# Kernel optimization log

Hardware: AMD Instinct MI355X
Metric: run time of the kernel (lower is better)

The kernel has to match this reference:

```python
import jax, jax.numpy as jnp
import numpy as np

INPUT_DIM, HIDDEN, OUT_DIM = 7, 64, 4


def _lstm_layer(x_seq, W_ih, W_hh, b_ih, b_hh):
    """Single LSTM layer, batch_first x_seq [B,T,D] -> [B,T,H]. PyTorch gate order i,f,g,o."""
    B = x_seq.shape[0]
    H = W_hh.shape[1]
    # Precompute input projection for all timesteps (hoist GEMM out of the scan).
    x_proj = jnp.einsum('btd,gd->btg', x_seq, W_ih) + b_ih + b_hh  # [B,T,4H]

    def step(carry, xt):
        h, c = carry
        gates = xt + h @ W_hh.T  # [B,4H]
        i, f, g, o = jnp.split(gates, 4, axis=-1)
        i = jax.nn.sigmoid(i)
        f = jax.nn.sigmoid(f)
        g = jnp.tanh(g)
        o = jax.nn.sigmoid(o)
        c = f * c + i * g
        h = o * jnp.tanh(c)
        return (h, c), h

    h0 = jnp.zeros((B, H), x_seq.dtype)
    c0 = jnp.zeros((B, H), x_seq.dtype)
    (_, _), hs = jax.lax.scan(step, (h0, c0), jnp.swapaxes(x_proj, 0, 1))  # hs [T,B,H]
    return jnp.swapaxes(hs, 0, 1)  # [B,T,H]


def setup_inputs() -> dict:
    key = jax.random.key(0)
    ks = jax.random.split(key, 12)
    s = 0.1  # init scale ~ 1/sqrt(hidden)
    x = jax.random.normal(ks[0], (4096, 512, INPUT_DIM), dtype=jnp.float32)
    W_ih0 = jax.random.normal(ks[1], (4 * HIDDEN, INPUT_DIM), dtype=jnp.float32) * s
    W_hh0 = jax.random.normal(ks[2], (4 * HIDDEN, HIDDEN), dtype=jnp.float32) * s
    b_ih0 = jax.random.normal(ks[3], (4 * HIDDEN,), dtype=jnp.float32) * s
    b_hh0 = jax.random.normal(ks[4], (4 * HIDDEN,), dtype=jnp.float32) * s
    W_ih1 = jax.random.normal(ks[5], (4 * HIDDEN, HIDDEN), dtype=jnp.float32) * s
    W_hh1 = jax.random.normal(ks[6], (4 * HIDDEN, HIDDEN), dtype=jnp.float32) * s
    b_ih1 = jax.random.normal(ks[7], (4 * HIDDEN,), dtype=jnp.float32) * s
    b_hh1 = jax.random.normal(ks[8], (4 * HIDDEN,), dtype=jnp.float32) * s
    W_fc = jax.random.normal(ks[9], (OUT_DIM, HIDDEN), dtype=jnp.float32) * s
    b_fc = jax.random.normal(ks[10], (OUT_DIM,), dtype=jnp.float32) * s
    return {"x": x, "W_ih0": W_ih0, "W_hh0": W_hh0, "b_ih0": b_ih0, "b_hh0": b_hh0,
            "W_ih1": W_ih1, "W_hh1": W_hh1, "b_ih1": b_ih1, "b_hh1": b_hh1,
            "W_fc": W_fc, "b_fc": b_fc}


def reference(x, W_ih0, W_hh0, b_ih0, b_hh0, W_ih1, W_hh1, b_ih1, b_hh1, W_fc, b_fc):
    h1 = _lstm_layer(x, W_ih0, W_hh0, b_ih0, b_hh0)   # [B,T,H]
    h2 = _lstm_layer(h1, W_ih1, W_hh1, b_ih1, b_hh1)  # [B,T,H]
    last = h2[:, -1, :]                               # [B,H]
    return last @ W_fc.T + b_fc                       # [B,4]
```

## Files before the change

kernel.cpp:

```cpp
#include <hip/hip_runtime.h>

#define T_SEQ 512
#define HID 64
#define MB 16
#define NTHREADS 1024
#define A1STR 104
#define A2STR 104

typedef __attribute__((ext_vector_type(8))) short short8;
typedef __attribute__((ext_vector_type(4))) float floatx4;

#define LOG2E 1.4426950408889634f

__device__ __forceinline__ short f2bf_rne(float v) {
  unsigned u = __float_as_uint(v);
  return (short)((u + 0x7FFFu + ((u >> 16) & 1u)) >> 16);
}
__device__ __forceinline__ float rcp_(float x) { return __builtin_amdgcn_rcpf(x); }
__device__ __forceinline__ float exp2_(float x) { return __builtin_amdgcn_exp2f(x); }

__device__ __forceinline__ float gate_h(const floatx4 p, float& c) {
  float A = exp2_(-p[0]);
  float F = exp2_(-p[1]);
  float G = exp2_(p[2]);
  float O = exp2_(-p[3]);
  float ig = (G - 1.f) * rcp_((1.f + A) * (G + 1.f));
  c = rcp_(1.f + F) * c + ig;
  float C = exp2_((2.f * LOG2E) * c);
  return (C - 1.f) * rcp_((1.f + O) * (C + 1.f));
}

__device__ __forceinline__ int uofp(int p) {
  return (p & ~7) + ((p & 7) >> 1) + ((p & 1) << 2);
}

__device__ __forceinline__ short w1elem(int k, int n, float wsc,
                                        const float* __restrict__ Wih0,
                                        const float* __restrict__ Whh0) {
  float v;
  if      (k < 64) { v = Whh0[n*64 + uofp(k)]; }
  else if (k < 71) { v = Wih0[n*7 + (k - 64)]; }
  else return (short)0;
  return f2bf_rne(v * wsc);
}
__device__ __forceinline__ short w2elem(int k, int n, float wsc,
                                        const float* __restrict__ Wih1,
                                        const float* __restrict__ Whh1) {
  float v;
  if (k < 64) { v = Wih1[n*64 + uofp(k)]; }
  else        { v = Whh1[n*64 + uofp(k - 64)]; }
  return f2bf_rne(v * wsc);
}

#define MFMA(A, B, C) __builtin_amdgcn_mfma_f32_16x16x32_bf16((A), (B), (C), 0, 0, 0)

#define PACK2(ha, hb)                                                        \
  ((unsigned)(unsigned short)f2bf_rne(ha) |                                  \
   ((unsigned)(unsigned short)f2bf_rne(hb) << 16))

__global__ __launch_bounds__(NTHREADS, 4) void lstm_fused(
    const float* __restrict__ x,
    const float* __restrict__ Wih0, const float* __restrict__ Whh0,
    const float* __restrict__ bih0, const float* __restrict__ bhh0,
    const float* __restrict__ Wih1, const float* __restrict__ Whh1,
    const float* __restrict__ bih1, const float* __restrict__ bhh1,
    const float* __restrict__ Wfc,  const float* __restrict__ bfc,
    float* __restrict__ out)
{
  __shared__ __align__(16) short A1[2][MB][A1STR];
  __shared__ __align__(16) short A2[2][MB][A2STR];
  __shared__ float h2f[MB][HID + 4];

  const int tid  = threadIdx.x;
  const int lane = tid & 63;
  const int wave = tid >> 6;
  const int wl   = wave & 7;
  const bool isL1 = wave < 8;
  const int l15  = lane & 15;
  const int quad = lane >> 4;
  const int quad8= quad * 8;
  const int g4   = l15 & 3;
  const int b0   = blockIdx.x * MB;
  const int u0   = wl*8 + quad;
  const int u1   = u0 + 4;
  const int hpos = wl*8 + 2*quad;
  const int n0   = g4*64 + (wl*8 + (l15 >> 2));
  const int n1   = n0 + 4;
  const float wsc = (g4 == 2) ? 2.f * LOG2E : LOG2E;

  for (int i = tid; i < 2*MB*A1STR/2; i += NTHREADS) ((unsigned*)A1)[i] = 0u;
  for (int i = tid; i < 2*MB*A2STR/2; i += NTHREADS) ((unsigned*)A2)[i] = 0u;

  const float* bi_ = isL1 ? bih0 : bih1;
  const float* bh_ = isL1 ? bhh0 : bhh1;
  floatx4 bia, bib;
  #pragma unroll
  for (int g = 0; g < 4; ++g) {
    float ws = (g == 2) ? 2.f * LOG2E : LOG2E;
    bia[g] = (bi_[g*64 + u0] + bh_[g*64 + u0]) * ws;
    bib[g] = (bi_[g*64 + u1] + bh_[g*64 + u1]) * ws;
  }

  const int xd   = lane & 31;
  const int xrow = 2*wl + (lane >> 5);
  const bool xact = isL1 && (xd < 7);
  const float* xbase = x + ((size_t)(b0 + xrow) * T_SEQ) * 7 + xd;
  float xcur = 0.f;
  if (xact) {
    A1[0][xrow][64 + xd] = f2bf_rne(xbase[0]);
    xcur = xbase[7];
  }

  short8 WA[4], WB[4];
  if (isL1) {
    #pragma unroll
    for (int ks = 0; ks < 3; ++ks) {
      short8 fa, fb;
      #pragma unroll
      for (int jj = 0; jj < 8; ++jj) {
        fa[jj] = w1elem(ks*32 + quad8 + jj, n0, wsc, Wih0, Whh0);
        fb[jj] = w1elem(ks*32 + quad8 + jj, n1, wsc, Wih0, Whh0);
      }
      WA[ks] = fa; WB[ks] = fb;
    }
  } else {
    #pragma unroll
    for (int ks = 0; ks < 4; ++ks) {
      short8 fa, fb;
      #pragma unroll
      for (int jj = 0; jj < 8; ++jj) {
        fa[jj] = w2elem(ks*32 + quad8 + jj, n0, wsc, Wih1, Whh1);
        fb[jj] = w2elem(ks*32 + quad8 + jj, n1, wsc, Wih1, Whh1);
      }
      WA[ks] = fa; WB[ks] = fb;
    }
  }
  __syncthreads();

  float ca = 0.f, cb = 0.f;

#define STEP_X(NXT, XT)                                                      \
    if (xact) {                                                              \
      A1[NXT][xrow][64 + xd] = f2bf_rne(xcur);                               \
      xcur = xbase[7 * (XT)];                                                \
    }

#define STEP_FULL(CUR, NXT, IT)                                              \
  {                                                                          \
    if (isL1) {                                                              \
      int xt_ = (IT) + 2; if (xt_ > T_SEQ - 1) xt_ = T_SEQ - 1;              \
      STEP_X(NXT, xt_)                                                       \
      short8 hf0 = *(const short8*)&A1[CUR][l15][     quad8];                \
      short8 hf1 = *(const short8*)&A1[CUR][l15][32 + quad8];                \
      short8 hfx = *(const short8*)&A1[CUR][l15][64 + quad8];                \
      floatx4 pa = bia, pb = bib;                                            \
      pa = MFMA(WA[0], hf0, pa);  pb = MFMA(WB[0], hf0, pb);                 \
      pa = MFMA(WA[1], hf1, pa);  pb = MFMA(WB[1], hf1, pb);                 \
      pa = MFMA(WA[2], hfx, pa);  pb = MFMA(WB[2], hfx, pb);                 \
      float ha = gate_h(pa, ca);                                             \
      float hb = gate_h(pb, cb);                                             \
      *(unsigned*)&A1[NXT][l15][hpos] = PACK2(ha, hb);                       \
    } else {                                                                 \
      short8 hf0 = *(const short8*)&A1[CUR][l15][     quad8];                \
      short8 hf1 = *(const short8*)&A1[CUR][l15][32 + quad8];                \
      short8 h20 = *(const short8*)&A2[CUR][l15][     quad8];                \
      short8 h21 = *(const short8*)&A2[CUR][l15][32 + quad8];                \
      floatx4 pa = bia, pb = bib;                                            \
      pa = MFMA(WA[0], hf0, pa);  pb = MFMA(WB[0], hf0, pb);                 \
      pa = MFMA(WA[1], hf1, pa);  pb = MFMA(WB[1], hf1, pb);                 \
      pa = MFMA(WA[2], h20, pa);  pb = MFMA(WB[2], h20, pb);                 \
      pa = MFMA(WA[3], h21, pa);  pb = MFMA(WB[3], h21, pb);                 \
      float ha = gate_h(pa, ca);                                             \
      float hb = gate_h(pb, cb);                                             \
      *(unsigned*)&A2[NXT][l15][hpos] = PACK2(ha, hb);                       \
    }                                                                        \
    __syncthreads();                                                         \
  }

  {
    if (isL1) {
      STEP_X(1, 2)
      short8 hf0 = *(const short8*)&A1[0][l15][     quad8];
      short8 hf1 = *(const short8*)&A1[0][l15][32 + quad8];
      short8 hfx = *(const short8*)&A1[0][l15][64 + quad8];
      floatx4 pa = bia, pb = bib;
      pa = MFMA(WA[0], hf0, pa);  pb = MFMA(WB[0], hf0, pb);
      pa = MFMA(WA[1], hf1, pa);  pb = MFMA(WB[1], hf1, pb);
      pa = MFMA(WA[2], hfx, pa);  pb = MFMA(WB[2], hfx, pb);
      float ha = gate_h(pa, ca);
      float hb = gate_h(pb, cb);
      *(unsigned*)&A1[1][l15][hpos] = PACK2(ha, hb);
    }
    __syncthreads();
  }

  #pragma unroll 1
  for (int k = 0; k < 255; ++k) {
    STEP_FULL(1, 0, 2*k + 1)
    STEP_FULL(0, 1, 2*k + 2)
  }
  STEP_FULL(1, 0, 511)

  {
    if (!isL1) {
      short8 hf0 = *(const short8*)&A1[0][l15][     quad8];
      short8 hf1 = *(const short8*)&A1[0][l15][32 + quad8];
      short8 h20 = *(const short8*)&A2[0][l15][     quad8];
      short8 h21 = *(const short8*)&A2[0][l15][32 + quad8];
      floatx4 pa = bia, pb = bib;
      pa = MFMA(WA[0], hf0, pa);  pb = MFMA(WB[0], hf0, pb);
      pa = MFMA(WA[1], hf1, pa);  pb = MFMA(WB[1], hf1, pb);
      pa = MFMA(WA[2], h20, pa);  pb = MFMA(WB[2], h20, pb);
      pa = MFMA(WA[3], h21, pa);  pb = MFMA(WB[3], h21, pb);
      h2f[l15][u0] = gate_h(pa, ca);
      h2f[l15][u1] = gate_h(pb, cb);
    }
    __syncthreads();
  }

  if (tid < MB * 4) {
    int bbf = tid >> 2, o = tid & 3;
    float acc = bfc[o];
    #pragma unroll 8
    for (int kk = 0; kk < HID; ++kk) acc += h2f[bbf][kk] * Wfc[o*HID + kk];
    out[(size_t)(b0 + bbf) * 4 + o] = acc;
  }
}

extern "C" void kernel_launch(void* const* d_in, const int* in_sizes, int n_in,
                              void* d_out, int out_size, void* d_ws, size_t ws_size,
                              hipStream_t stream) {
  const float* x    = (const float*)d_in[0];
  const float* Wih0 = (const float*)d_in[1];
  const float* Whh0 = (const float*)d_in[2];
  const float* bih0 = (const float*)d_in[3];
  const float* bhh0 = (const float*)d_in[4];
  const float* Wih1 = (const float*)d_in[5];
  const float* Whh1 = (const float*)d_in[6];
  const float* bih1 = (const float*)d_in[7];
  const float* bhh1 = (const float*)d_in[8];
  const float* Wfc  = (const float*)d_in[9];
  const float* bfc  = (const float*)d_in[10];
  (void)d_ws; (void)ws_size; (void)n_in; (void)out_size;

  const int B = in_sizes[0] / (T_SEQ * 7);
  dim3 grid(B / MB);
  lstm_fused<<<grid, NTHREADS, 0, stream>>>(x, Wih0, Whh0, bih0, bhh0,
                                            Wih1, Whh1, bih1, bhh1, Wfc, bfc,
                                            (float*)d_out);
}
```

Measured before the change: 438.5 us.

## Merge layer-1 and layer-2 waves so each wave computes both LSTM layers

```diff
diff --git a/kernel.cpp b/kernel.cpp
--- a/kernel.cpp
+++ b/kernel.cpp
@@ -3,7 +3,7 @@
 #define T_SEQ 512
 #define HID 64
 #define MB 16
-#define NTHREADS 1024
+#define NTHREADS 512
 #define A1STR 104
 #define A2STR 104
 
@@ -74,36 +74,34 @@
   const int tid  = threadIdx.x;
   const int lane = tid & 63;
   const int wave = tid >> 6;
-  const int wl   = wave & 7;
-  const bool isL1 = wave < 8;
   const int l15  = lane & 15;
   const int quad = lane >> 4;
   const int quad8= quad * 8;
   const int g4   = l15 & 3;
   const int b0   = blockIdx.x * MB;
-  const int u0   = wl*8 + quad;
+  const int u0   = wave*8 + quad;
   const int u1   = u0 + 4;
-  const int hpos = wl*8 + 2*quad;
-  const int n0   = g4*64 + (wl*8 + (l15 >> 2));
+  const int hpos = wave*8 + 2*quad;
+  const int n0   = g4*64 + (wave*8 + (l15 >> 2));
   const int n1   = n0 + 4;
   const float wsc = (g4 == 2) ? 2.f * LOG2E : LOG2E;
 
   for (int i = tid; i < 2*MB*A1STR/2; i += NTHREADS) ((unsigned*)A1)[i] = 0u;
   for (int i = tid; i < 2*MB*A2STR/2; i += NTHREADS) ((unsigned*)A2)[i] = 0u;
 
-  const float* bi_ = isL1 ? bih0 : bih1;
-  const float* bh_ = isL1 ? bhh0 : bhh1;
-  floatx4 bia, bib;
+  floatx4 b1a, b1b, b2a, b2b;
   #pragma unroll
   for (int g = 0; g < 4; ++g) {
     float ws = (g == 2) ? 2.f * LOG2E : LOG2E;
-    bia[g] = (bi_[g*64 + u0] + bh_[g*64 + u0]) * ws;
-    bib[g] = (bi_[g*64 + u1] + bh_[g*64 + u1]) * ws;
+    b1a[g] = (bih0[g*64 + u0] + bhh0[g*64 + u0]) * ws;
+    b1b[g] = (bih0[g*64 + u1] + bhh0[g*64 + u1]) * ws;
+    b2a[g] = (bih1[g*64 + u0] + bhh1[g*64 + u0]) * ws;
+    b2b[g] = (bih1[g*64 + u1] + bhh1[g*64 + u1]) * ws;
   }
 
   const int xd   = lane & 31;
-  const int xrow = 2*wl + (lane >> 5);
-  const bool xact = isL1 && (xd < 7);
+  const int xrow = 2*wave + (lane >> 5);
+  const bool xact = (xd < 7);
   const float* xbase = x + ((size_t)(b0 + xrow) * T_SEQ) * 7 + xd;
   float xcur = 0.f;
   if (xact) {
@@ -111,33 +109,30 @@
     xcur = xbase[7];
   }
 
-  short8 WA[4], WB[4];
-  if (isL1) {
+  short8 W1f[3][2], W2f[4][2];
+  #pragma unroll
+  for (int ks = 0; ks < 3; ++ks) {
+    short8 fa, fb;
     #pragma unroll
-    for (int ks = 0; ks < 3; ++ks) {
-      short8 fa, fb;
-      #pragma unroll
-      for (int jj = 0; jj < 8; ++jj) {
-        fa[jj] = w1elem(ks*32 + quad8 + jj, n0, wsc, Wih0, Whh0);
-        fb[jj] = w1elem(ks*32 + quad8 + jj, n1, wsc, Wih0, Whh0);
-      }
-      WA[ks] = fa; WB[ks] = fb;
+    for (int jj = 0; jj < 8; ++jj) {
+      fa[jj] = w1elem(ks*32 + quad8 + jj, n0, wsc, Wih0, Whh0);
+      fb[jj] = w1elem(ks*32 + quad8 + jj, n1, wsc, Wih0, Whh0);
     }
-  } else {
+    W1f[ks][0] = fa; W1f[ks][1] = fb;
+  }
+  #pragma unroll
+  for (int ks = 0; ks < 4; ++ks) {
+    short8 fa, fb;
     #pragma unroll
-    for (int ks = 0; ks < 4; ++ks) {
-      short8 fa, fb;
-      #pragma unroll
-      for (int jj = 0; jj < 8; ++jj) {
-        fa[jj] = w2elem(ks*32 + quad8 + jj, n0, wsc, Wih1, Whh1);
-        fb[jj] = w2elem(ks*32 + quad8 + jj, n1, wsc, Wih1, Whh1);
-      }
-      WA[ks] = fa; WB[ks] = fb;
+    for (int jj = 0; jj < 8; ++jj) {
+      fa[jj] = w2elem(ks*32 + quad8 + jj, n0, wsc, Wih1, Whh1);
+      fb[jj] = w2elem(ks*32 + quad8 + jj, n1, wsc, Wih1, Whh1);
     }
+    W2f[ks][0] = fa; W2f[ks][1] = fb;
   }
   __syncthreads();
 
-  float ca = 0.f, cb = 0.f;
+  float c1a = 0.f, c1b = 0.f, c2a = 0.f, c2b = 0.f;
 
 #define STEP_X(NXT, XT)                                                      \
     if (xact) {                                                              \
@@ -147,50 +142,46 @@
 
 #define STEP_FULL(CUR, NXT, IT)                                              \
   {                                                                          \
-    if (isL1) {                                                              \
-      int xt_ = (IT) + 2; if (xt_ > T_SEQ - 1) xt_ = T_SEQ - 1;              \
-      STEP_X(NXT, xt_)                                                       \
-      short8 hf0 = *(const short8*)&A1[CUR][l15][     quad8];                \
-      short8 hf1 = *(const short8*)&A1[CUR][l15][32 + quad8];                \
-      short8 hfx = *(const short8*)&A1[CUR][l15][64 + quad8];                \
-      floatx4 pa = bia, pb = bib;                                            \
-      pa = MFMA(WA[0], hf0, pa);  pb = MFMA(WB[0], hf0, pb);                 \
-      pa = MFMA(WA[1], hf1, pa);  pb = MFMA(WB[1], hf1, pb);                 \
-      pa = MFMA(WA[2], hfx, pa);  pb = MFMA(WB[2], hfx, pb);                 \
-      float ha = gate_h(pa, ca);                                             \
-      float hb = gate_h(pb, cb);                                             \
+    int xt_ = (IT) + 2; if (xt_ > T_SEQ - 1) xt_ = T_SEQ - 1;                \
+    STEP_X(NXT, xt_)                                                         \
+    short8 hf0 = *(const short8*)&A1[CUR][l15][     quad8];                  \
+    short8 hf1 = *(const short8*)&A1[CUR][l15][32 + quad8];                  \
+    short8 hfx = *(const short8*)&A1[CUR][l15][64 + quad8];                  \
+    short8 h20 = *(const short8*)&A2[CUR][l15][     quad8];                  \
+    short8 h21 = *(const short8*)&A2[CUR][l15][32 + quad8];                  \
+    floatx4 pa = b1a, pb = b1b, qa = b2a, qb = b2b;                          \
+    pa = MFMA(W1f[0][0], hf0, pa);  pb = MFMA(W1f[0][1], hf0, pb);           \
+    qa = MFMA(W2f[0][0], hf0, qa);  qb = MFMA(W2f[0][1], hf0, qb);           \
+    pa = MFMA(W1f[1][0], hf1, pa);  pb = MFMA(W1f[1][1], hf1, pb);           \
+    qa = MFMA(W2f[1][0], hf1, qa);  qb = MFMA(W2f[1][1], hf1, qb);           \
+    pa = MFMA(W1f[2][0], hfx, pa);  pb = MFMA(W1f[2][1], hfx, pb);           \
+    qa = MFMA(W2f[2][0], h20, qa);  qb = MFMA(W2f[2][1], h20, qb);           \
+    qa = MFMA(W2f[3][0], h21, qa);  qb = MFMA(W2f[3][1], h21, qb);           \
+    {                                                                        \
+      float ha = gate_h(pa, c1a);                                            \
+      float hb = gate_h(pb, c1b);                                            \
       *(unsigned*)&A1[NXT][l15][hpos] = PACK2(ha, hb);                       \
-    } else {                                                                 \
-      short8 hf0 = *(const short8*)&A1[CUR][l15][     quad8];                \
-      short8 hf1 = *(const short8*)&A1[CUR][l15][32 + quad8];                \
-      short8 h20 = *(const short8*)&A2[CUR][l15][     quad8];                \
-      short8 h21 = *(const short8*)&A2[CUR][l15][32 + quad8];                \
-      floatx4 pa = bia, pb = bib;                                            \
-      pa = MFMA(WA[0], hf0, pa);  pb = MFMA(WB[0], hf0, pb);                 \
-      pa = MFMA(WA[1], hf1, pa);  pb = MFMA(WB[1], hf1, pb);                 \
-      pa = MFMA(WA[2], h20, pa);  pb = MFMA(WB[2], h20, pb);                 \
-      pa = MFMA(WA[3], h21, pa);  pb = MFMA(WB[3], h21, pb);                 \
-      float ha = gate_h(pa, ca);                                             \
-      float hb = gate_h(pb, cb);                                             \
+    }                                                                        \
+    {                                                                        \
+      float ha = gate_h(qa, c2a);                                            \
+      float hb = gate_h(qb, c2b);                                            \
       *(unsigned*)&A2[NXT][l15][hpos] = PACK2(ha, hb);                       \
     }                                                                        \
     __syncthreads();                                                         \
   }
 
   {
-    if (isL1) {
-      STEP_X(1, 2)
-      short8 hf0 = *(const short8*)&A1[0][l15][     quad8];
-      short8 hf1 = *(const short8*)&A1[0][l15][32 + quad8];
-      short8 hfx = *(const short8*)&A1[0][l15][64 + quad8];
-      floatx4 pa = bia, pb = bib;
-      pa = MFMA(WA[0], hf0, pa);  pb = MFMA(WB[0], hf0, pb);
-      pa = MFMA(WA[1], hf1, pa);  pb = MFMA(WB[1], hf1, pb);
-      pa = MFMA(WA[2], hfx, pa);  pb = MFMA(WB[2], hfx, pb);
-      float ha = gate_h(pa, ca);
-      float hb = gate_h(pb, cb);
-      *(unsigned*)&A1[1][l15][hpos] = PACK2(ha, hb);
-    }
+    STEP_X(1, 2)
+    short8 hf0 = *(const short8*)&A1[0][l15][     quad8];
+    short8 hf1 = *(const short8*)&A1[0][l15][32 + quad8];
+    short8 hfx = *(const short8*)&A1[0][l15][64 + quad8];
+    floatx4 pa = b1a, pb = b1b;
+    pa = MFMA(W1f[0][0], hf0, pa);  pb = MFMA(W1f[0][1], hf0, pb);
+    pa = MFMA(W1f[1][0], hf1, pa);  pb = MFMA(W1f[1][1], hf1, pb);
+    pa = MFMA(W1f[2][0], hfx, pa);  pb = MFMA(W1f[2][1], hfx, pb);
+    float ha = gate_h(pa, c1a);
+    float hb = gate_h(pb, c1b);
+    *(unsigned*)&A1[1][l15][hpos] = PACK2(ha, hb);
     __syncthreads();
   }
 
@@ -202,19 +193,17 @@
   STEP_FULL(1, 0, 511)
 
   {
-    if (!isL1) {
-      short8 hf0 = *(const short8*)&A1[0][l15][     quad8];
-      short8 hf1 = *(const short8*)&A1[0][l15][32 + quad8];
-      short8 h20 = *(const short8*)&A2[0][l15][     quad8];
-      short8 h21 = *(const short8*)&A2[0][l15][32 + quad8];
-      floatx4 pa = bia, pb = bib;
-      pa = MFMA(WA[0], hf0, pa);  pb = MFMA(WB[0], hf0, pb);
-      pa = MFMA(WA[1], hf1, pa);  pb = MFMA(WB[1], hf1, pb);
-      pa = MFMA(WA[2], h20, pa);  pb = MFMA(WB[2], h20, pb);
-      pa = MFMA(WA[3], h21, pa);  pb = MFMA(WB[3], h21, pb);
-      h2f[l15][u0] = gate_h(pa, ca);
-      h2f[l15][u1] = gate_h(pb, cb);
-    }
+    short8 hf0 = *(const short8*)&A1[0][l15][     quad8];
+    short8 hf1 = *(const short8*)&A1[0][l15][32 + quad8];
+    short8 h20 = *(const short8*)&A2[0][l15][     quad8];
+    short8 h21 = *(const short8*)&A2[0][l15][32 + quad8];
+    floatx4 qa = b2a, qb = b2b;
+    qa = MFMA(W2f[0][0], hf0, qa);  qb = MFMA(W2f[0][1], hf0, qb);
+    qa = MFMA(W2f[1][0], hf1, qa);  qb = MFMA(W2f[1][1], hf1, qb);
+    qa = MFMA(W2f[2][0], h20, qa);  qb = MFMA(W2f[2][1], h20, qb);
+    qa = MFMA(W2f[3][0], h21, qa);  qb = MFMA(W2f[3][1], h21, qb);
+    h2f[l15][u0] = gate_h(qa, c2a);
+    h2f[l15][u1] = gate_h(qb, c2b);
     __syncthreads();
   }
 
```

Result: slower. 490.9 us (+12.0%).
